# Kernel optimization log

Hardware: AMD Instinct MI355X
Metric: run time of the kernel (lower is better)

The kernel has to match this reference:

```python
import jax, jax.numpy as jnp
import numpy as np

# dims
B, F, K = 64, 4096, 8
D_IN = D_SLOT = D_KVQ = 192
HID = 768
N_ITERS = 3
EPS = 1e-8
GROUPS = [(0, 1), (1, 7), (7, 8)]  # bg / fg / ag contiguous slot slices
SB_STRENGTH = 1.0
SB_SIGMA = 0.25
GRID = 64  # sqrt(F)


def _layernorm(x, g, b):
    m = jnp.mean(x, axis=-1, keepdims=True)
    v = jnp.mean(jnp.square(x - m), axis=-1, keepdims=True)
    return (x - m) * jax.lax.rsqrt(v + 1e-5) * g + b


def _gru_cell(x, h, Wih, Whh, bih, bhh):
    # torch.nn.GRUCell semantics; gate order r, z, n
    gi = x @ Wih.T + bih
    gh = h @ Whh.T + bhh
    ir, iz, i_n = jnp.split(gi, 3, axis=-1)
    hr, hz, h_n = jnp.split(gh, 3, axis=-1)
    r = jax.nn.sigmoid(ir + hr)
    z = jax.nn.sigmoid(iz + hz)
    n = jnp.tanh(i_n + r * h_n)
    return (1.0 - z) * n + z * h


def _token_coords():
    y = np.linspace(-1.0, 1.0, GRID, dtype=np.float32)
    x = np.linspace(-1.0, 1.0, GRID, dtype=np.float32)
    yy, xx = np.meshgrid(y, x, indexing='ij')
    return jnp.asarray(np.stack((xx, yy), axis=-1).reshape(F, 2))


def setup_inputs() -> dict:
    key = jax.random.key(0)
    ks = jax.random.split(key, 16)
    def n(i, shape, s=0.02):
        return jax.random.normal(ks[i], shape, jnp.float32) * s
    return dict(
        features=jax.random.normal(ks[0], (B, F, D_IN), jnp.float32),
        slots=jax.random.normal(ks[1], (B, K, D_SLOT), jnp.float32),
        Wk=n(2, (D_IN, D_KVQ)), Wv=n(3, (D_IN, D_KVQ)), Wq=n(4, (D_SLOT, D_KVQ)),
        ln_feat_g=jnp.ones(D_IN), ln_feat_b=jnp.zeros(D_IN),
        ln_slot_g=jnp.ones(D_SLOT), ln_slot_b=jnp.zeros(D_SLOT),
        gru_Wih=n(5, (3, 3 * D_SLOT, D_KVQ)), gru_Whh=n(6, (3, 3 * D_SLOT, D_SLOT)),
        gru_bih=n(7, (3, 3 * D_SLOT)), gru_bhh=n(8, (3, 3 * D_SLOT)),
        mlp_ln_g=jnp.ones((3, D_SLOT)), mlp_ln_b=jnp.zeros((3, D_SLOT)),
        mlp_W1=n(9, (3, D_SLOT, HID)), mlp_b1=n(10, (3, HID)),
        mlp_W2=n(11, (3, HID, D_SLOT)), mlp_b2=n(12, (3, D_SLOT)),
    )


def reference(features, slots, Wk, Wv, Wq, ln_feat_g, ln_feat_b, ln_slot_g,
              ln_slot_b, gru_Wih, gru_Whh, gru_bih, gru_bhh, mlp_ln_g,
              mlp_ln_b, mlp_W1, mlp_b1, mlp_W2, mlp_b2):
    coords = _token_coords()  # (F, 2)
    f = _layernorm(features, ln_feat_g, ln_feat_b)
    k = f @ Wk  # (B, F, Dk)
    v = f @ Wv
    scale = D_KVQ ** -0.5
    sigma2 = max(SB_SIGMA ** 2, 1e-8)
    prev_attn = None
    for _ in range(N_ITERS):
        slots_prev = slots
        q = _layernorm(slots, ln_slot_g, ln_slot_b) @ Wq  # (B, K, Dk)
        dots = jnp.einsum('bkd,bfd->bkf', q, k) * scale
        if prev_attn is not None and SB_STRENGTH > 0.0:
            w = prev_attn / (prev_attn.sum(-1, keepdims=True) + 1e-8)
            centers = jnp.einsum('bkf,fd->bkd', w, coords)  # (B, K, 2)
            diff = coords[None, None] - centers[:, :, None]  # (B, K, F, 2)
            dist2 = jnp.sum(diff * diff, axis=-1)
            dots = dots + SB_STRENGTH * (-dist2 / (2.0 * sigma2))
        attn = jax.nn.softmax(dots, axis=1)  # competition over slots
        prev_attn = attn
        w = attn / (attn.sum(-1, keepdims=True) + EPS)  # weighted mean over F
        updates = jnp.einsum('bkf,bfd->bkd', w, v)  # (B, K, Dk)
        outs = []
        for g, (s, e) in enumerate(GROUPS):
            u = updates[:, s:e].reshape(-1, D_KVQ)
            h_prev = slots_prev[:, s:e].reshape(-1, D_SLOT)
            h = _gru_cell(u, h_prev, gru_Wih[g], gru_Whh[g], gru_bih[g], gru_bhh[g])
            x = _layernorm(h, mlp_ln_g[g], mlp_ln_b[g])
            x = jax.nn.relu(x @ mlp_W1[g] + mlp_b1[g]) @ mlp_W2[g] + mlp_b2[g]
            outs.append((h + x).reshape(B, e - s, D_SLOT))
        slots = jnp.concatenate(outs, axis=1)
    return slots
```

## Files before the change

kernel.cpp:

```cpp
#include <hip/hip_runtime.h>

typedef unsigned short u16;
typedef unsigned int u32;

#define BB 64
#define FF 4096
#define DD 192
#define HH 768

typedef __attribute__((ext_vector_type(8))) __bf16 bf16x8;
typedef __attribute__((ext_vector_type(4))) float f32x4;

__device__ __forceinline__ float bf2f(u32 u) {
  union { u32 i; float f; } x; x.i = u << 16; return x.f;
}
__device__ __forceinline__ u16 f2bf(float f) {
  union { u32 i; float f; } x; x.f = f;
  return (u16)((x.i + 0x7fffu + ((x.i >> 16) & 1u)) >> 16);
}
__device__ __forceinline__ float sigm(float x) { return 1.f / (1.f + __expf(-x)); }

__global__ void prep_wmod(const float* __restrict__ Wk, const float* __restrict__ Wv,
                          const float* __restrict__ g, const float* __restrict__ bb,
                          u16* __restrict__ wmodT, float* __restrict__ s1,
                          float* __restrict__ s0) {
  int n = blockIdx.x * 64 + threadIdx.x;
  const float* W = (n < DD) ? Wk : Wv;
  int col = (n < DD) ? n : n - DD;
  float a1 = 0.f, a0 = 0.f;
  for (int e = 0; e < DD; ++e) {
    float w = W[e * DD + col];
    u16 h = f2bf(g[e] * w);
    wmodT[n * DD + e] = h;
    a1 += bf2f(h);
    a0 += bb[e] * w;
  }
  s1[n] = a1; s0[n] = a0;
}

__global__ void prep_packw(const float* __restrict__ Wih, const float* __restrict__ Whh,
                           const float* __restrict__ W1, const float* __restrict__ W2,
                           u16* __restrict__ pWih, u16* __restrict__ pWhh,
                           u16* __restrict__ pW1, u16* __restrict__ pW2) {
  int which = blockIdx.y;
  int total, N, E;
  const float* src; u16* dst; int srcEmajor;
  if (which < 2) { total = 3 * 576 * 192; N = 576; E = 192; srcEmajor = 0;
                   src = which ? Whh : Wih; dst = which ? pWhh : pWih; }
  else if (which == 2) { total = 3 * 192 * 768; N = 768; E = 192; srcEmajor = 1;
                         src = W1; dst = pW1; }
  else { total = 3 * 768 * 192; N = 192; E = 768; srcEmajor = 1; src = W2; dst = pW2; }
  for (int idx = blockIdx.x * 256 + threadIdx.x; idx < total; idx += gridDim.x * 256) {
    int g = idx / (N * E), rem = idx % (N * E);
    int n, e;
    if (srcEmajor) { e = rem / N; n = rem % N; }
    else { n = rem / E; e = rem % E; }
    dst[((g * (E / 2) + (e >> 1)) * N + n) * 2 + (e & 1)] = f2bf(src[idx]);
  }
}

__global__ __launch_bounds__(512) void proj_kernel(
    const float* __restrict__ feat, const u16* __restrict__ wmodT,
    const float* __restrict__ s1, const float* __restrict__ s0,
    u16* __restrict__ kc_, u16* __restrict__ vT) {
  __shared__ __align__(16) u16 Atile[128 * 192];
  __shared__ float stats[128 * 2];
  int tid = threadIdx.x;
  long tile_base = (long)blockIdx.x * 128;
  int w = tid >> 6, lane = tid & 63;
  {
    int r = w * 16 + (lane >> 2);
    int p = lane & 3;
    const float4* src = (const float4*)(feat + (tile_base + r) * DD) + p * 12;
    float s = 0.f, s2 = 0.f;
    #pragma unroll
    for (int i = 0; i < 12; ++i) {
      float4 v = src[i];
      s += v.x + v.y + v.z + v.w;
      s2 += v.x * v.x + v.y * v.y + v.z * v.z + v.w * v.w;
      uint2 pk;
      pk.x = (u32)f2bf(v.x) | ((u32)f2bf(v.y) << 16);
      pk.y = (u32)f2bf(v.z) | ((u32)f2bf(v.w) << 16);
      int u = p * 6 + (i >> 1);
      *(uint2*)((char*)Atile + r * 384 + ((u ^ (r & 7)) << 4) + (i & 1) * 8) = pk;
    }
    s += __shfl_xor(s, 1); s2 += __shfl_xor(s2, 1);
    s += __shfl_xor(s, 2); s2 += __shfl_xor(s2, 2);
    if (p == 0) {
      float mu = s * (1.f / 192.f);
      stats[r * 2] = mu;
      stats[r * 2 + 1] = rsqrtf(s2 * (1.f / 192.f) - mu * mu + 1e-5f);
    }
  }
  __syncthreads();
  int mh = w >> 2, nq = w & 3;
  int l15 = lane & 15, l4 = lane >> 4;
  f32x4 acc[4][6];
  #pragma unroll
  for (int a = 0; a < 4; ++a)
    #pragma unroll
    for (int b2 = 0; b2 < 6; ++b2) acc[a][b2] = (f32x4){0.f, 0.f, 0.f, 0.f};
  #pragma unroll
  for (int kk = 0; kk < 6; ++kk) {
    bf16x8 afr[4];
    #pragma unroll
    for (int mt = 0; mt < 4; ++mt) {
      int row = mh * 64 + mt * 16 + l15;
      int u = kk * 4 + l4;
      afr[mt] = *(bf16x8*)((char*)Atile + row * 384 + ((u ^ (row & 7)) << 4));
    }
    bf16x8 bfr[6];
    #pragma unroll
    for (int nt = 0; nt < 6; ++nt) {
      int col = nq * 96 + nt * 16 + l15;
      bfr[nt] = *(const bf16x8*)(wmodT + col * DD + kk * 32 + l4 * 8);
    }
    #pragma unroll
    for (int mt = 0; mt < 4; ++mt)
      #pragma unroll
      for (int nt = 0; nt < 6; ++nt)
        acc[mt][nt] = __builtin_amdgcn_mfma_f32_16x16x32_bf16(afr[mt], bfr[nt],
                                                              acc[mt][nt], 0, 0, 0);
  }
  float muv[4][4], rsv[4][4];
  #pragma unroll
  for (int mt = 0; mt < 4; ++mt)
    #pragma unroll
    for (int j = 0; j < 4; ++j) {
      int row = mh * 64 + mt * 16 + l4 * 4 + j;
      muv[mt][j] = stats[row * 2];
      rsv[mt][j] = stats[row * 2 + 1];
    }
  __syncthreads();
  if (nq < 2) {
    #pragma unroll
    for (int nt = 0; nt < 6; ++nt) {
      int col = nq * 96 + nt * 16 + l15;
      float s1c = s1[col], s0c = s0[col];
      int u = col >> 3, ce = (col & 7) * 2;
      #pragma unroll
      for (int mt = 0; mt < 4; ++mt) {
        #pragma unroll
        for (int j = 0; j < 4; ++j) {
          int row = mh * 64 + mt * 16 + l4 * 4 + j;
          u16 hv = f2bf(rsv[mt][j] * (acc[mt][nt][j] - muv[mt][j] * s1c) + s0c);
          *(u16*)((char*)Atile + row * 384 + ((u ^ (row & 7)) << 4) + ce) = hv;
        }
      }
    }
  }
  __syncthreads();
  {
    long Tg0 = tile_base >> 4;
    #pragma unroll
    for (int p2 = 0; p2 < 6; ++p2) {
      int fi = tid + p2 * 512;
      int tau = fi & 15, u = (fi >> 4) % 24, tt = fi / 384;
      uint4 val = *(uint4*)((char*)Atile + (tt * 16 + tau) * 384 + ((u ^ (tau & 7)) << 4));
      *(uint4*)(kc_ + (((Tg0 + tt) * 24 + u) * 16 + tau) * 8) = val;
    }
  }
  __syncthreads();
  if (nq >= 2) {
    #pragma unroll
    for (int nt = 0; nt < 6; ++nt) {
      int col = nq * 96 + nt * 16 + l15;
      float s1c = s1[col], s0c = s0[col];
      int vcol = col - 192;
      #pragma unroll
      for (int mt = 0; mt < 4; ++mt) {
        int tok0 = mh * 64 + mt * 16 + l4 * 4;
        u16 h[4];
        #pragma unroll
        for (int j = 0; j < 4; ++j)
          h[j] = f2bf(rsv[mt][j] * (acc[mt][nt][j] - muv[mt][j] * s1c) + s0c);
        uint2 pk;
        pk.x = (u32)h[0] | ((u32)h[1] << 16);
        pk.y = (u32)h[2] | ((u32)h[3] << 16);
        *(uint2*)((char*)Atile + vcol * 256 + (((tok0 >> 3) ^ (vcol & 7)) << 4) +
                  (tok0 & 7) * 2) = pk;
      }
    }
  }
  __syncthreads();
  {
    long bidx = tile_base / FF;
    int f0 = (int)(tile_base % FF);
    #pragma unroll
    for (int p2 = 0; p2 < 6; ++p2) {
      int fi = tid + p2 * 512;
      int d = fi >> 4, tc = fi & 15;
      uint4 val = *(uint4*)((char*)Atile + d * 256 + ((tc ^ (d & 7)) << 4));
      *(uint4*)(vT + (bidx * 192 + d) * FF + f0 + tc * 8) = val;
    }
  }
}

__global__ __launch_bounds__(64) void qproj_kernel(
    const float* __restrict__ slots, const float* __restrict__ Wq,
    const float* __restrict__ g, const float* __restrict__ bb,
    float* __restrict__ qbuf) {
  __shared__ float ln[192];
  int bk = blockIdx.x;
  int lane = threadIdx.x;
  const float* x = slots + bk * DD;
  float v0 = x[lane], v1 = x[lane + 64], v2 = x[lane + 128];
  float s = v0 + v1 + v2, s2 = v0 * v0 + v1 * v1 + v2 * v2;
  #pragma unroll
  for (int m = 1; m < 64; m <<= 1) { s += __shfl_xor(s, m); s2 += __shfl_xor(s2, m); }
  float mu = s * (1.f / 192.f);
  float rstd = rsqrtf(s2 * (1.f / 192.f) - mu * mu + 1e-5f);
  ln[lane]       = (v0 - mu) * rstd * g[lane]       + bb[lane];
  ln[lane + 64]  = (v1 - mu) * rstd * g[lane + 64]  + bb[lane + 64];
  ln[lane + 128] = (v2 - mu) * rstd * g[lane + 128] + bb[lane + 128];
  __syncthreads();
  float a0 = 0.f, a1 = 0.f, a2 = 0.f;
  for (int e = 0; e < DD; ++e) {
    float le = ln[e];
    a0 += le * Wq[e * DD + lane];
    a1 += le * Wq[e * DD + lane + 64];
    a2 += le * Wq[e * DD + lane + 128];
  }
  const float scale = 0.07216878364870323f;
  qbuf[bk * DD + lane]       = a0 * scale;
  qbuf[bk * DD + lane + 64]  = a1 * scale;
  qbuf[bk * DD + lane + 128] = a2 * scale;
}

__global__ __launch_bounds__(256) void attn_kernel(
    const u16* __restrict__ kc_, const float* __restrict__ qbuf,
    const float* __restrict__ asum_prev, const float* __restrict__ cacc_prev,
    u16* __restrict__ attnT, float* __restrict__ asum_cur,
    float* __restrict__ cacc_cur, int have_bias) {
  __shared__ __align__(16) u16 qlds[16 * 192];
  int b = blockIdx.x;
  int chunk = blockIdx.y * 256;
  int tid = threadIdx.x;
  if (tid < 192) {
    int s = tid / 24, u = tid % 24;
    const float* qp = qbuf + (b * 8 + s) * DD + u * 8;
    uint4 p;
    p.x = (u32)f2bf(qp[0]) | ((u32)f2bf(qp[1]) << 16);
    p.y = (u32)f2bf(qp[2]) | ((u32)f2bf(qp[3]) << 16);
    p.z = (u32)f2bf(qp[4]) | ((u32)f2bf(qp[5]) << 16);
    p.w = (u32)f2bf(qp[6]) | ((u32)f2bf(qp[7]) << 16);
    *(uint4*)((char*)qlds + s * 384 + ((u ^ (s & 7)) << 4)) = p;
  } else {
    int t2 = tid - 192;
    #pragma unroll
    for (int i = 0; i < 3; ++i) {
      int idx = t2 * 3 + i;
      int s = 8 + idx / 24, u = idx % 24;
      *(uint4*)((char*)qlds + s * 384 + ((u ^ (s & 7)) << 4)) = (uint4){0, 0, 0, 0};
    }
  }
  __syncthreads();
  int w = tid >> 6, lane = tid & 63;
  int l15 = lane & 15, l4 = lane >> 4;
  bf16x8 qfr[6];
  #pragma unroll
  for (int kk = 0; kk < 6; ++kk) {
    int u = kk * 4 + l4;
    qfr[kk] = *(bf16x8*)((char*)qlds + l15 * 384 + ((u ^ (l15 & 7)) << 4));
  }
  float ax[4], ay[4], c0[4];
  #pragma unroll
  for (int j = 0; j < 4; ++j) {
    int s = l4 * 4 + j;
    if (have_bias && s < 8) {
      float inv = 1.f / (asum_prev[b * 8 + s] + 1e-8f);
      float cx = cacc_prev[(b * 8 + s) * 2] * inv;
      float cy = cacc_prev[(b * 8 + s) * 2 + 1] * inv;
      ax[j] = 16.f * cx; ay[j] = 16.f * cy; c0[j] = -8.f * (cx * cx + cy * cy);
    } else { ax[j] = 0.f; ay[j] = 0.f; c0[j] = 0.f; }
  }
  float pa[4], px[4], py[4];
  #pragma unroll
  for (int j = 0; j < 4; ++j) { pa[j] = 0.f; px[j] = 0.f; py[j] = 0.f; }
  for (int tile = w; tile < 16; tile += 4) {
    int t0 = chunk + tile * 16;
    long Tg = (long)b * 256 + (t0 >> 4);
    const u16* kp = kc_ + (Tg * 24 + l4) * 128 + l15 * 8;
    f32x4 acc = (f32x4){0.f, 0.f, 0.f, 0.f};
    #pragma unroll
    for (int kk = 0; kk < 6; ++kk) {
      bf16x8 bfr = *(const bf16x8*)(kp + kk * 512);
      acc = __builtin_amdgcn_mfma_f32_16x16x32_bf16(qfr[kk], bfr, acc, 0, 0, 0);
    }
    int t = t0 + l15;
    float x = -1.f + (float)(t & 63) * (2.f / 63.f);
    float y = -1.f + (float)(t >> 6) * (2.f / 63.f);
    float m8r2 = -8.f * (x * x + y * y);
    float d4[4];
    #pragma unroll
    for (int j = 0; j < 4; ++j)
      d4[j] = acc[j] + (have_bias ? (ax[j] * x + ay[j] * y + c0[j] + m8r2) : 0.f);
    float o4[4];
    #pragma unroll
    for (int j = 0; j < 4; ++j) o4[j] = __shfl_xor(d4[j], 16);
    float mx = fmaxf(fmaxf(fmaxf(d4[0], d4[1]), fmaxf(d4[2], d4[3])),
                     fmaxf(fmaxf(o4[0], o4[1]), fmaxf(o4[2], o4[3])));
    float e4[4];
    float sum = 0.f;
    #pragma unroll
    for (int j = 0; j < 4; ++j) { e4[j] = __expf(d4[j] - mx); sum += e4[j]; }
    #pragma unroll
    for (int j = 0; j < 4; ++j) sum += __expf(o4[j] - mx);
    float inv = 1.f / sum;
    if (l4 < 2) {
      #pragma unroll
      for (int j = 0; j < 4; ++j) {
        float a = e4[j] * inv;
        attnT[((long)(b * 16) + l4 * 4 + j) * FF + t] = f2bf(a);
        pa[j] += a; px[j] += a * x; py[j] += a * y;
      }
    }
  }
  #pragma unroll
  for (int m = 1; m < 16; m <<= 1) {
    #pragma unroll
    for (int j = 0; j < 4; ++j) {
      pa[j] += __shfl_xor(pa[j], m);
      px[j] += __shfl_xor(px[j], m);
      py[j] += __shfl_xor(py[j], m);
    }
  }
  if (l15 == 0 && l4 < 2) {
    #pragma unroll
    for (int j = 0; j < 4; ++j) {
      int s = l4 * 4 + j;
      atomicAdd(&asum_cur[b * 8 + s], pa[j]);
      atomicAdd(&cacc_cur[(b * 8 + s) * 2], px[j]);
      atomicAdd(&cacc_cur[(b * 8 + s) * 2 + 1], py[j]);
    }
  }
}

__global__ __launch_bounds__(256) void upd_kernel(
    const u16* __restrict__ attnT, const u16* __restrict__ vT,
    float* __restrict__ upd) {
  __shared__ float red[4][8][16];
  int b = blockIdx.x, nt = blockIdx.y;
  int tid = threadIdx.x;
  int w = tid >> 6, lane = tid & 63;
  int l15 = lane & 15, l4 = lane >> 4;
  int kc = w * 1024;
  const u16* ap = attnT + ((long)(b * 16) + l15) * FF + kc + l4 * 8;
  const u16* vp = vT + ((long)b * 192 + nt * 16 + l15) * FF + kc + l4 * 8;
  f32x4 acc = (f32x4){0.f, 0.f, 0.f, 0.f};
  #pragma unroll 4
  for (int ks = 0; ks < 32; ++ks) {
    bf16x8 afr = *(const bf16x8*)(ap + ks * 32);
    bf16x8 bfr = *(const bf16x8*)(vp + ks * 32);
    acc = __builtin_amdgcn_mfma_f32_16x16x32_bf16(afr, bfr, acc, 0, 0, 0);
  }
  if (l4 < 2) {
    #pragma unroll
    for (int j = 0; j < 4; ++j) red[w][l4 * 4 + j][l15] = acc[j];
  }
  __syncthreads();
  if (tid < 128) {
    int s = tid >> 4, l = tid & 15;
    float t = red[0][s][l] + red[1][s][l] + red[2][s][l] + red[3][s][l];
    upd[((long)b * 8 + s) * DD + nt * 16 + l] = t;
  }
}

template <int M>
__device__ void gru_body(int b0, int g, int srow,
                         float* u_l, float* h_l, float* gi_l, float* gh_l,
                         float* hn_l, float* ln_l, float* x1_l, float* out_l, float* st,
                         const float* __restrict__ upd, const float* __restrict__ asum,
                         const float* __restrict__ sin_,
                         const u16* __restrict__ pWih, const u16* __restrict__ pWhh,
                         const float* __restrict__ bih, const float* __restrict__ bhh,
                         const float* __restrict__ mlng, const float* __restrict__ mlnb,
                         const u16* __restrict__ pW1, const float* __restrict__ b1,
                         const u16* __restrict__ pW2, const float* __restrict__ b2,
                         float* __restrict__ sout) {
  int tid = threadIdx.x;
  for (int idx = tid; idx < M * 192; idx += 768) {
    int row = idx / 192, d = idx % 192;
    int gr = b0 * 8 + srow + row;
    float inv = 1.f / (asum[gr] + 1e-8f);
    u_l[row * 192 + d] = upd[gr * DD + d] * inv;
    h_l[row * 192 + d] = sin_[gr * DD + d];
  }
  __syncthreads();
  if (tid < 576) {
    int c = tid;
    const u16* wih = pWih + (size_t)g * 96 * 1152 + c * 2;
    const u16* whh = pWhh + (size_t)g * 96 * 1152 + c * 2;
    float ai[M], ah[M];
    #pragma unroll
    for (int r = 0; r < M; ++r) { ai[r] = 0.f; ah[r] = 0.f; }
    #pragma unroll 4
    for (int e2 = 0; e2 < 96; ++e2) {
      u32 wi = *(const u32*)(wih + e2 * 1152);
      u32 wh = *(const u32*)(whh + e2 * 1152);
      float wi0 = bf2f(wi & 0xffffu), wi1 = bf2f(wi >> 16);
      float wh0 = bf2f(wh & 0xffffu), wh1 = bf2f(wh >> 16);
      #pragma unroll
      for (int r = 0; r < M; ++r) {
        ai[r] += wi0 * u_l[r * 192 + e2 * 2] + wi1 * u_l[r * 192 + e2 * 2 + 1];
        ah[r] += wh0 * h_l[r * 192 + e2 * 2] + wh1 * h_l[r * 192 + e2 * 2 + 1];
      }
    }
    #pragma unroll
    for (int r = 0; r < M; ++r) { gi_l[r * 576 + c] = ai[r]; gh_l[r * 576 + c] = ah[r]; }
  }
  __syncthreads();
  if (tid < M * 192) {
    int row = tid / 192, uu = tid % 192;
    const float* bihg = bih + g * 576;
    const float* bhhg = bhh + g * 576;
    float r_ = sigm(gi_l[row * 576 + uu] + bihg[uu] + gh_l[row * 576 + uu] + bhhg[uu]);
    float z_ = sigm(gi_l[row * 576 + 192 + uu] + bihg[192 + uu] +
                    gh_l[row * 576 + 192 + uu] + bhhg[192 + uu]);
    float nn = gi_l[row * 576 + 384 + uu] + bihg[384 + uu] +
               r_ * (gh_l[row * 576 + 384 + uu] + bhhg[384 + uu]);
    float t = 1.f - 2.f / (__expf(2.f * nn) + 1.f);
    hn_l[row * 192 + uu] = (1.f - z_) * t + z_ * h_l[row * 192 + uu];
  }
  __syncthreads();
  {
    int wv = tid >> 6, lane = tid & 63;
    if (wv < M) {
      float v0 = hn_l[wv * 192 + lane], v1 = hn_l[wv * 192 + lane + 64],
            v2 = hn_l[wv * 192 + lane + 128];
      float s = v0 + v1 + v2, sq = v0 * v0 + v1 * v1 + v2 * v2;
      #pragma unroll
      for (int m = 1; m < 64; m <<= 1) { s += __shfl_xor(s, m); sq += __shfl_xor(sq, m); }
      if (lane == 0) {
        float mu = s * (1.f / 192.f);
        st[wv * 2] = mu;
        st[wv * 2 + 1] = rsqrtf(sq * (1.f / 192.f) - mu * mu + 1e-5f);
      }
    }
  }
  __syncthreads();
  if (tid < M * 192) {
    int row = tid / 192, uu = tid % 192;
    ln_l[row * 192 + uu] = (hn_l[row * 192 + uu] - st[row * 2]) * st[row * 2 + 1] *
                               mlng[g * DD + uu] + mlnb[g * DD + uu];
  }
  __syncthreads();
  {
    int c = tid;
    const u16* w1 = pW1 + (size_t)g * 96 * 1536 + c * 2;
    float a[M];
    #pragma unroll
    for (int r = 0; r < M; ++r) a[r] = 0.f;
    #pragma unroll 4
    for (int e2 = 0; e2 < 96; ++e2) {
      u32 wp = *(const u32*)(w1 + e2 * 1536);
      float w0 = bf2f(wp & 0xffffu), w1f = bf2f(wp >> 16);
      #pragma unroll
      for (int r = 0; r < M; ++r)
        a[r] += w0 * ln_l[r * 192 + e2 * 2] + w1f * ln_l[r * 192 + e2 * 2 + 1];
    }
    float bc = b1[g * HH + c];
    #pragma unroll
    for (int r = 0; r < M; ++r) x1_l[r * 768 + c] = fmaxf(a[r] + bc, 0.f);
  }
  if (tid < M * 192) {
    int row = tid / 192, uu = tid % 192;
    out_l[row * 192 + uu] = hn_l[row * 192 + uu] + b2[g * DD + uu];
  }
  __syncthreads();
  {
    int c = tid % 192, ks = tid / 192;
    const u16* w2 = pW2 + (size_t)g * 384 * 384 + c * 2;
    float a[M];
    #pragma unroll
    for (int r = 0; r < M; ++r) a[r] = 0.f;
    #pragma unroll 4
    for (int e2 = ks * 96; e2 < ks * 96 + 96; ++e2) {
      u32 wp = *(const u32*)(w2 + e2 * 384);
      float w0 = bf2f(wp & 0xffffu), w1f = bf2f(wp >> 16);
      #pragma unroll
      for (int r = 0; r < M; ++r)
        a[r] += w0 * x1_l[r * 768 + e2 * 2] + w1f * x1_l[r * 768 + e2 * 2 + 1];
    }
    #pragma unroll
    for (int r = 0; r < M; ++r) atomicAdd(&out_l[r * 192 + c], a[r]);
  }
  __syncthreads();
  if (tid < M * 192) {
    int row = tid / 192, d = tid % 192;
    sout[(b0 * 8 + srow + row) * DD + d] = out_l[row * 192 + d];
  }
}

__global__ __launch_bounds__(768) void gru_kernel(
    const float* __restrict__ upd, const float* __restrict__ asum,
    const float* __restrict__ sin_,
    const u16* __restrict__ pWih, const u16* __restrict__ pWhh,
    const float* __restrict__ bih, const float* __restrict__ bhh,
    const float* __restrict__ mlng, const float* __restrict__ mlnb,
    const u16* __restrict__ pW1, const float* __restrict__ b1,
    const u16* __restrict__ pW2, const float* __restrict__ b2,
    float* __restrict__ sout) {
  __shared__ float u_l[3 * 192], h_l[3 * 192], gi_l[3 * 576], gh_l[3 * 576];
  __shared__ float hn_l[3 * 192], ln_l[3 * 192], x1_l[3 * 768], out_l[3 * 192], st[8];
  int b = blockIdx.x, y = blockIdx.y;
  if (y == 0)
    gru_body<1>(b, 0, 0, u_l, h_l, gi_l, gh_l, hn_l, ln_l, x1_l, out_l, st,
                upd, asum, sin_, pWih, pWhh, bih, bhh, mlng, mlnb, pW1, b1, pW2, b2, sout);
  else if (y == 1)
    gru_body<1>(b, 2, 7, u_l, h_l, gi_l, gh_l, hn_l, ln_l, x1_l, out_l, st,
                upd, asum, sin_, pWih, pWhh, bih, bhh, mlng, mlnb, pW1, b1, pW2, b2, sout);
  else if (y == 2)
    gru_body<3>(b, 1, 1, u_l, h_l, gi_l, gh_l, hn_l, ln_l, x1_l, out_l, st,
                upd, asum, sin_, pWih, pWhh, bih, bhh, mlng, mlnb, pW1, b1, pW2, b2, sout);
  else
    gru_body<3>(b, 1, 4, u_l, h_l, gi_l, gh_l, hn_l, ln_l, x1_l, out_l, st,
                upd, asum, sin_, pWih, pWhh, bih, bhh, mlng, mlnb, pW1, b1, pW2, b2, sout);
}

extern "C" void kernel_launch(void* const* d_in, const int* in_sizes, int n_in,
                              void* d_out, int out_size, void* d_ws, size_t ws_size,
                              hipStream_t stream) {
  const float* feat = (const float*)d_in[0];
  const float* slots = (const float*)d_in[1];
  const float* Wk = (const float*)d_in[2];
  const float* Wv = (const float*)d_in[3];
  const float* Wq = (const float*)d_in[4];
  const float* lfg = (const float*)d_in[5];
  const float* lfb = (const float*)d_in[6];
  const float* lsg = (const float*)d_in[7];
  const float* lsb = (const float*)d_in[8];
  const float* gWih = (const float*)d_in[9];
  const float* gWhh = (const float*)d_in[10];
  const float* gbih = (const float*)d_in[11];
  const float* gbhh = (const float*)d_in[12];
  const float* mlng = (const float*)d_in[13];
  const float* mlnb = (const float*)d_in[14];
  const float* W1 = (const float*)d_in[15];
  const float* b1 = (const float*)d_in[16];
  const float* W2 = (const float*)d_in[17];
  const float* b2 = (const float*)d_in[18];
  float* out = (float*)d_out;

  char* ws = (char*)d_ws;
  size_t off = 0;
  auto alloc = [&](size_t bytes) {
    void* p = ws + off;
    off += (bytes + 255) & ~(size_t)255;
    return p;
  };
  u16* kc_    = (u16*)alloc((size_t)BB * FF * DD * 2);
  u16* vT     = (u16*)alloc((size_t)BB * DD * FF * 2);
  u16* attnT  = (u16*)alloc((size_t)BB * 16 * FF * 2);
  float* qbuf = (float*)alloc((size_t)BB * 8 * DD * 4);
  float* upd  = (float*)alloc((size_t)BB * 8 * DD * 4);
  float* slA  = (float*)alloc((size_t)BB * 8 * DD * 4);
  float* slB  = (float*)alloc((size_t)BB * 8 * DD * 4);
  float* asum0 = (float*)alloc(BB * 8 * 4);
  float* asum1 = (float*)alloc(BB * 8 * 4);
  float* cacc0 = (float*)alloc(BB * 8 * 2 * 4);
  float* cacc1 = (float*)alloc(BB * 8 * 2 * 4);
  u16* wmodT  = (u16*)alloc(384 * DD * 2);
  float* s1   = (float*)alloc(384 * 4);
  float* s0   = (float*)alloc(384 * 4);
  u16* pWih   = (u16*)alloc((size_t)3 * 576 * DD * 2);
  u16* pWhh   = (u16*)alloc((size_t)3 * 576 * DD * 2);
  u16* pW1    = (u16*)alloc((size_t)3 * DD * HH * 2);
  u16* pW2    = (u16*)alloc((size_t)3 * HH * DD * 2);

  prep_wmod<<<6, 64, 0, stream>>>(Wk, Wv, lfg, lfb, wmodT, s1, s0);
  prep_packw<<<dim3(432, 4), 256, 0, stream>>>(gWih, gWhh, W1, W2, pWih, pWhh, pW1, pW2);
  proj_kernel<<<BB * FF / 128, 512, 0, stream>>>(feat, wmodT, s1, s0, kc_, vT);

  const float* sin_ = slots;
  float* souts[3] = {slA, slB, out};
  float* asums[2] = {asum0, asum1};
  float* caccs[2] = {cacc0, cacc1};
  for (int it = 0; it < 3; ++it) {
    int cur = it & 1, prev = cur ^ 1;
    hipMemsetAsync(asums[cur], 0, BB * 8 * 4, stream);
    hipMemsetAsync(caccs[cur], 0, BB * 8 * 2 * 4, stream);
    qproj_kernel<<<BB * 8, 64, 0, stream>>>(sin_, Wq, lsg, lsb, qbuf);
    attn_kernel<<<dim3(BB, 16), 256, 0, stream>>>(kc_, qbuf, asums[prev], caccs[prev],
                                                  attnT, asums[cur], caccs[cur], it > 0 ? 1 : 0);
    upd_kernel<<<dim3(BB, 12), 256, 0, stream>>>(attnT, vT, upd);
    gru_kernel<<<dim3(BB, 4), 768, 0, stream>>>(upd, asums[cur], sin_, pWih, pWhh,
                                                gbih, gbhh, mlng, mlnb, pW1, b1, pW2, b2,
                                                souts[it]);
    sin_ = souts[it];
  }
}
```

Measured before the change: 548.4 us.

## Fuse attention with update matmul and write V in MFMA-ready packed layout

Merges the attention-softmax kernel and the update matmul into one kernel. Attention weights now stay in shared memory instead of making a global round trip, and partial updates are accumulated with atomicAdd into a buffer that is zeroed each iteration. The projection kernel now writes V directly from registers in a blocked layout that feeds MFMA loads, using a cross-lane shuffle in place of an LDS transpose. It also shrinks the projection tile to 64 rows and 256 threads, and switches to the native bf16 conversion. In exchange there are float atomics on the update buffer, which make the summation order nondeterministic, plus an extra memset per iteration.

```diff
diff --git a/kernel.cpp b/kernel.cpp
--- a/kernel.cpp
+++ b/kernel.cpp
@@ -15,8 +15,11 @@
   union { u32 i; float f; } x; x.i = u << 16; return x.f;
 }
 __device__ __forceinline__ u16 f2bf(float f) {
-  union { u32 i; float f; } x; x.f = f;
-  return (u16)((x.i + 0x7fffu + ((x.i >> 16) & 1u)) >> 16);
+  __bf16 h = (__bf16)f;
+  return __builtin_bit_cast(u16, h);
+}
+__device__ __forceinline__ u32 pk2bf(float a, float b) {
+  return (u32)f2bf(a) | ((u32)f2bf(b) << 16);
 }
 __device__ __forceinline__ float sigm(float x) { return 1.f / (1.f + __expf(-x)); }
 
@@ -59,14 +62,14 @@
   }
 }
 
-__global__ __launch_bounds__(512) void proj_kernel(
+__global__ __launch_bounds__(256, 4) void proj_kernel(
     const float* __restrict__ feat, const u16* __restrict__ wmodT,
     const float* __restrict__ s1, const float* __restrict__ s0,
-    u16* __restrict__ kc_, u16* __restrict__ vT) {
-  __shared__ __align__(16) u16 Atile[128 * 192];
-  __shared__ float stats[128 * 2];
+    u16* __restrict__ kc_, u16* __restrict__ vc_) {
+  __shared__ __align__(16) u16 Atile[64 * 192];
+  __shared__ float stats[64 * 2];
   int tid = threadIdx.x;
-  long tile_base = (long)blockIdx.x * 128;
+  long tile_base = (long)blockIdx.x * 64;
   int w = tid >> 6, lane = tid & 63;
   {
     int r = w * 16 + (lane >> 2);
@@ -79,8 +82,8 @@
       s += v.x + v.y + v.z + v.w;
       s2 += v.x * v.x + v.y * v.y + v.z * v.z + v.w * v.w;
       uint2 pk;
-      pk.x = (u32)f2bf(v.x) | ((u32)f2bf(v.y) << 16);
-      pk.y = (u32)f2bf(v.z) | ((u32)f2bf(v.w) << 16);
+      pk.x = pk2bf(v.x, v.y);
+      pk.y = pk2bf(v.z, v.w);
       int u = p * 6 + (i >> 1);
       *(uint2*)((char*)Atile + r * 384 + ((u ^ (r & 7)) << 4) + (i & 1) * 8) = pk;
     }
@@ -93,7 +96,6 @@
     }
   }
   __syncthreads();
-  int mh = w >> 2, nq = w & 3;
   int l15 = lane & 15, l4 = lane >> 4;
   f32x4 acc[4][6];
   #pragma unroll
@@ -105,14 +107,14 @@
     bf16x8 afr[4];
     #pragma unroll
     for (int mt = 0; mt < 4; ++mt) {
-      int row = mh * 64 + mt * 16 + l15;
+      int row = mt * 16 + l15;
       int u = kk * 4 + l4;
       afr[mt] = *(bf16x8*)((char*)Atile + row * 384 + ((u ^ (row & 7)) << 4));
     }
     bf16x8 bfr[6];
     #pragma unroll
     for (int nt = 0; nt < 6; ++nt) {
-      int col = nq * 96 + nt * 16 + l15;
+      int col = w * 96 + nt * 16 + l15;
       bfr[nt] = *(const bf16x8*)(wmodT + col * DD + kk * 32 + l4 * 8);
     }
     #pragma unroll
@@ -127,71 +129,65 @@
   for (int mt = 0; mt < 4; ++mt)
     #pragma unroll
     for (int j = 0; j < 4; ++j) {
-      int row = mh * 64 + mt * 16 + l4 * 4 + j;
+      int row = mt * 16 + l4 * 4 + j;
       muv[mt][j] = stats[row * 2];
       rsv[mt][j] = stats[row * 2 + 1];
     }
   __syncthreads();
-  if (nq < 2) {
+  long bidx = tile_base / FF;
+  int f0 = (int)(tile_base % FF);
+  if (w < 2) {
     #pragma unroll
     for (int nt = 0; nt < 6; ++nt) {
-      int col = nq * 96 + nt * 16 + l15;
+      int col = w * 96 + nt * 16 + l15;
       float s1c = s1[col], s0c = s0[col];
       int u = col >> 3, ce = (col & 7) * 2;
       #pragma unroll
       for (int mt = 0; mt < 4; ++mt) {
         #pragma unroll
         for (int j = 0; j < 4; ++j) {
-          int row = mh * 64 + mt * 16 + l4 * 4 + j;
+          int row = mt * 16 + l4 * 4 + j;
           u16 hv = f2bf(rsv[mt][j] * (acc[mt][nt][j] - muv[mt][j] * s1c) + s0c);
           *(u16*)((char*)Atile + row * 384 + ((u ^ (row & 7)) << 4) + ce) = hv;
         }
       }
     }
+  } else {
+    #pragma unroll
+    for (int nt = 0; nt < 6; ++nt) {
+      int col = (w - 2) * 96 + nt * 16 + l15;
+      float s1c = s1[col + 192], s0c = s0[col + 192];
+      int ntg = col >> 4;
+      #pragma unroll
+      for (int mt = 0; mt < 4; ++mt) {
+        int tl = mt * 16 + l4 * 4;
+        uint2 pk;
+        pk.x = pk2bf(rsv[mt][0] * (acc[mt][nt][0] - muv[mt][0] * s1c) + s0c,
+                     rsv[mt][1] * (acc[mt][nt][1] - muv[mt][1] * s1c) + s0c);
+        pk.y = pk2bf(rsv[mt][2] * (acc[mt][nt][2] - muv[mt][2] * s1c) + s0c,
+                     rsv[mt][3] * (acc[mt][nt][3] - muv[mt][3] * s1c) + s0c);
+        u32 ox = __shfl_xor((int)pk.x, 16);
+        u32 oy = __shfl_xor((int)pk.y, 16);
+        if ((l4 & 1) == 0) {
+          int t0 = f0 + tl;
+          int g32 = t0 >> 5;
+          int l4f = (t0 >> 3) & 3;
+          uint4 val = {pk.x, pk.y, ox, oy};
+          *(uint4*)(vc_ + ((((long)bidx * 128 + g32) * 12 + ntg) * 64 + l4f * 16 +
+                           (col & 15)) * 8) = val;
+        }
+      }
+    }
   }
   __syncthreads();
   {
     long Tg0 = tile_base >> 4;
     #pragma unroll
     for (int p2 = 0; p2 < 6; ++p2) {
-      int fi = tid + p2 * 512;
+      int fi = tid + p2 * 256;
       int tau = fi & 15, u = (fi >> 4) % 24, tt = fi / 384;
       uint4 val = *(uint4*)((char*)Atile + (tt * 16 + tau) * 384 + ((u ^ (tau & 7)) << 4));
       *(uint4*)(kc_ + (((Tg0 + tt) * 24 + u) * 16 + tau) * 8) = val;
-    }
-  }
-  __syncthreads();
-  if (nq >= 2) {
-    #pragma unroll
-    for (int nt = 0; nt < 6; ++nt) {
-      int col = nq * 96 + nt * 16 + l15;
-      float s1c = s1[col], s0c = s0[col];
-      int vcol = col - 192;
-      #pragma unroll
-      for (int mt = 0; mt < 4; ++mt) {
-        int tok0 = mh * 64 + mt * 16 + l4 * 4;
-        u16 h[4];
-        #pragma unroll
-        for (int j = 0; j < 4; ++j)
-          h[j] = f2bf(rsv[mt][j] * (acc[mt][nt][j] - muv[mt][j] * s1c) + s0c);
-        uint2 pk;
-        pk.x = (u32)h[0] | ((u32)h[1] << 16);
-        pk.y = (u32)h[2] | ((u32)h[3] << 16);
-        *(uint2*)((char*)Atile + vcol * 256 + (((tok0 >> 3) ^ (vcol & 7)) << 4) +
-                  (tok0 & 7) * 2) = pk;
-      }
-    }
-  }
-  __syncthreads();
-  {
-    long bidx = tile_base / FF;
-    int f0 = (int)(tile_base % FF);
-    #pragma unroll
-    for (int p2 = 0; p2 < 6; ++p2) {
-      int fi = tid + p2 * 512;
-      int d = fi >> 4, tc = fi & 15;
-      uint4 val = *(uint4*)((char*)Atile + d * 256 + ((tc ^ (d & 7)) << 4));
-      *(uint4*)(vT + (bidx * 192 + d) * FF + f0 + tc * 8) = val;
     }
   }
 }
@@ -227,12 +223,14 @@
   qbuf[bk * DD + lane + 128] = a2 * scale;
 }
 
-__global__ __launch_bounds__(256) void attn_kernel(
-    const u16* __restrict__ kc_, const float* __restrict__ qbuf,
+__global__ __launch_bounds__(256) void attnupd_kernel(
+    const u16* __restrict__ kc_, const u16* __restrict__ vc_,
+    const float* __restrict__ qbuf,
     const float* __restrict__ asum_prev, const float* __restrict__ cacc_prev,
-    u16* __restrict__ attnT, float* __restrict__ asum_cur,
+    float* __restrict__ upd, float* __restrict__ asum_cur,
     float* __restrict__ cacc_cur, int have_bias) {
   __shared__ __align__(16) u16 qlds[16 * 192];
+  __shared__ __align__(16) u16 attn_lds[16 * 256];
   int b = blockIdx.x;
   int chunk = blockIdx.y * 256;
   int tid = threadIdx.x;
@@ -240,10 +238,10 @@
     int s = tid / 24, u = tid % 24;
     const float* qp = qbuf + (b * 8 + s) * DD + u * 8;
     uint4 p;
-    p.x = (u32)f2bf(qp[0]) | ((u32)f2bf(qp[1]) << 16);
-    p.y = (u32)f2bf(qp[2]) | ((u32)f2bf(qp[3]) << 16);
-    p.z = (u32)f2bf(qp[4]) | ((u32)f2bf(qp[5]) << 16);
-    p.w = (u32)f2bf(qp[6]) | ((u32)f2bf(qp[7]) << 16);
+    p.x = pk2bf(qp[0], qp[1]);
+    p.y = pk2bf(qp[2], qp[3]);
+    p.z = pk2bf(qp[4], qp[5]);
+    p.w = pk2bf(qp[6], qp[7]);
     *(uint4*)((char*)qlds + s * 384 + ((u ^ (s & 7)) << 4)) = p;
   } else {
     int t2 = tid - 192;
@@ -253,6 +251,9 @@
       int s = 8 + idx / 24, u = idx % 24;
       *(uint4*)((char*)qlds + s * 384 + ((u ^ (s & 7)) << 4)) = (uint4){0, 0, 0, 0};
     }
+    #pragma unroll
+    for (int i = 0; i < 4; ++i)
+      *(uint4*)((char*)attn_lds + 4096 + (t2 * 4 + i) * 16) = (uint4){0, 0, 0, 0};
   }
   __syncthreads();
   int w = tid >> 6, lane = tid & 63;
@@ -308,10 +309,12 @@
     for (int j = 0; j < 4; ++j) sum += __expf(o4[j] - mx);
     float inv = 1.f / sum;
     if (l4 < 2) {
+      int tl = tile * 16 + l15;
       #pragma unroll
       for (int j = 0; j < 4; ++j) {
         float a = e4[j] * inv;
-        attnT[((long)(b * 16) + l4 * 4 + j) * FF + t] = f2bf(a);
+        int s = l4 * 4 + j;
+        *(u16*)((char*)attn_lds + ((s * 512 + tl * 2) ^ ((s & 7) << 4))) = f2bf(a);
         pa[j] += a; px[j] += a * x; py[j] += a * y;
       }
     }
@@ -334,35 +337,27 @@
       atomicAdd(&cacc_cur[(b * 8 + s) * 2 + 1], py[j]);
     }
   }
-}
-
-__global__ __launch_bounds__(256) void upd_kernel(
-    const u16* __restrict__ attnT, const u16* __restrict__ vT,
-    float* __restrict__ upd) {
-  __shared__ float red[4][8][16];
-  int b = blockIdx.x, nt = blockIdx.y;
-  int tid = threadIdx.x;
-  int w = tid >> 6, lane = tid & 63;
-  int l15 = lane & 15, l4 = lane >> 4;
-  int kc = w * 1024;
-  const u16* ap = attnT + ((long)(b * 16) + l15) * FF + kc + l4 * 8;
-  const u16* vp = vT + ((long)b * 192 + nt * 16 + l15) * FF + kc + l4 * 8;
-  f32x4 acc = (f32x4){0.f, 0.f, 0.f, 0.f};
-  #pragma unroll 4
-  for (int ks = 0; ks < 32; ++ks) {
-    bf16x8 afr = *(const bf16x8*)(ap + ks * 32);
-    bf16x8 bfr = *(const bf16x8*)(vp + ks * 32);
-    acc = __builtin_amdgcn_mfma_f32_16x16x32_bf16(afr, bfr, acc, 0, 0, 0);
-  }
-  if (l4 < 2) {
-    #pragma unroll
-    for (int j = 0; j < 4; ++j) red[w][l4 * 4 + j][l15] = acc[j];
-  }
-  __syncthreads();
-  if (tid < 128) {
-    int s = tid >> 4, l = tid & 15;
-    float t = red[0][s][l] + red[1][s][l] + red[2][s][l] + red[3][s][l];
-    upd[((long)b * 8 + s) * DD + nt * 16 + l] = t;
+  __syncthreads();
+  int g32base = chunk >> 5;
+  #pragma unroll
+  for (int ni = 0; ni < 3; ++ni) {
+    int nt = w * 3 + ni;
+    f32x4 acc = (f32x4){0.f, 0.f, 0.f, 0.f};
+    const u16* vp = vc_ + ((((long)b * 128 + g32base) * 12 + nt) * 64 + l4 * 16 + l15) * 8;
+    #pragma unroll
+    for (int gl = 0; gl < 8; ++gl) {
+      int tl0 = gl * 32 + l4 * 8;
+      bf16x8 afr = *(bf16x8*)((char*)attn_lds + ((l15 * 512 + tl0 * 2) ^ ((l15 & 7) << 4)));
+      bf16x8 bfr = *(const bf16x8*)(vp + gl * 12 * 64 * 8);
+      acc = __builtin_amdgcn_mfma_f32_16x16x32_bf16(afr, bfr, acc, 0, 0, 0);
+    }
+    if (l4 < 2) {
+      #pragma unroll
+      for (int j = 0; j < 4; ++j) {
+        int s = l4 * 4 + j;
+        atomicAdd(&upd[((long)b * 8 + s) * DD + nt * 16 + l15], acc[j]);
+      }
+    }
   }
 }
 
@@ -550,8 +545,7 @@
     return p;
   };
   u16* kc_    = (u16*)alloc((size_t)BB * FF * DD * 2);
-  u16* vT     = (u16*)alloc((size_t)BB * DD * FF * 2);
-  u16* attnT  = (u16*)alloc((size_t)BB * 16 * FF * 2);
+  u16* vc_    = (u16*)alloc((size_t)BB * DD * FF * 2);
   float* qbuf = (float*)alloc((size_t)BB * 8 * DD * 4);
   float* upd  = (float*)alloc((size_t)BB * 8 * DD * 4);
   float* slA  = (float*)alloc((size_t)BB * 8 * DD * 4);
@@ -570,7 +564,7 @@
 
   prep_wmod<<<6, 64, 0, stream>>>(Wk, Wv, lfg, lfb, wmodT, s1, s0);
   prep_packw<<<dim3(432, 4), 256, 0, stream>>>(gWih, gWhh, W1, W2, pWih, pWhh, pW1, pW2);
-  proj_kernel<<<BB * FF / 128, 512, 0, stream>>>(feat, wmodT, s1, s0, kc_, vT);
+  proj_kernel<<<BB * FF / 64, 256, 0, stream>>>(feat, wmodT, s1, s0, kc_, vc_);
 
   const float* sin_ = slots;
   float* souts[3] = {slA, slB, out};
@@ -578,12 +572,13 @@
   float* caccs[2] = {cacc0, cacc1};
   for (int it = 0; it < 3; ++it) {
     int cur = it & 1, prev = cur ^ 1;
+    hipMemsetAsync(upd, 0, BB * 8 * DD * 4, stream);
     hipMemsetAsync(asums[cur], 0, BB * 8 * 4, stream);
     hipMemsetAsync(caccs[cur], 0, BB * 8 * 2 * 4, stream);
     qproj_kernel<<<BB * 8, 64, 0, stream>>>(sin_, Wq, lsg, lsb, qbuf);
-    attn_kernel<<<dim3(BB, 16), 256, 0, stream>>>(kc_, qbuf, asums[prev], caccs[prev],
-                                                  attnT, asums[cur], caccs[cur], it > 0 ? 1 : 0);
-    upd_kernel<<<dim3(BB, 12), 256, 0, stream>>>(attnT, vT, upd);
+    attnupd_kernel<<<dim3(BB, 16), 256, 0, stream>>>(kc_, vc_, qbuf, asums[prev],
+                                                     caccs[prev], upd, asums[cur],
+                                                     caccs[cur], it > 0 ? 1 : 0);
     gru_kernel<<<dim3(BB, 4), 768, 0, stream>>>(upd, asums[cur], sin_, pWih, pWhh,
                                                 gbih, gbhh, mlng, mlnb, pW1, b1, pW2, b2,
                                                 souts[it]);
```

After: 646.7 us. 17.9% more time.
